# Performance work log

Hardware: AMD Instinct MI355X
Metric: run time of the kernel (lower is better)

Reference implementation:

```python
import jax, jax.numpy as jnp
import numpy as np

N = 100000      # nodes
E = 3200000     # edges (avg degree 32)
D = 256         # feature dim
C = 40          # classes
KEEP = 0.5      # 1 - dropout


def setup_inputs() -> dict:
    key = jax.random.key(0)
    k1, k2, k3, k4, k5, k6, k7 = jax.random.split(key, 7)
    x = jax.random.normal(k1, (N, D), dtype=jnp.float32)
    adj_row = jnp.sort(jax.random.randint(k2, (E,), 0, N))
    adj_col = jax.random.randint(k3, (E,), 0, N)
    # roughly degree-normalized edge weights (~1/avg_degree scale)
    adj_vals = jax.random.uniform(k4, (E,), dtype=jnp.float32) * (2.0 / 32.0)
    W = jax.random.normal(k5, (C, D), dtype=jnp.float32) * (1.0 / np.sqrt(D))
    b = jax.random.normal(k6, (C,), dtype=jnp.float32) * 0.01
    # precomputed dropout keep-mask (training mode, p=0.5)
    drop_mask = (jax.random.uniform(k7, (N, D)) < KEEP).astype(jnp.float32)
    return {"x": x, "adj_vals": adj_vals, "W": W, "b": b,
            "drop_mask": drop_mask, "adj_row": adj_row, "adj_col": adj_col}


def reference(x, adj_vals, W, b, drop_mask, adj_row, adj_col):
    n = x.shape[0]

    def spmm(v):  # sparse [N,N] @ dense [N,d] via gather + segment-sum
        return jax.ops.segment_sum(adj_vals[:, None] * v[adj_col], adj_row,
                                   num_segments=n)

    # hidden GraphConvolution (use_linear=False): spmm -> relu -> dropout
    h = jax.nn.relu(spmm(x))
    h = h * drop_mask / KEEP
    # gc_class: Linear(D->C) then spmm
    out = spmm(h @ W.T + b)  # [N, C]
    return out
```

## Files before the change

### kernel.cpp

```cpp
#include <hip/hip_runtime.h>

#define NN 100000
#define EE 3200000
#define DD 256
#define CC 40
#define NCH 8
#define CH 32
#define UN2 8

#define CAPW 640
#define COHORT 256
#define CHUNK_BLOCKS (COHORT * 8)
#define WPC (COHORT * 4)
#define WG16 (NN / 16)
#define LROWS 64

__device__ __forceinline__ float bf2f(unsigned int u) {
    return __uint_as_float(u << 16);
}
__device__ __forceinline__ unsigned short f2bf(float f) {
    unsigned int t = __float_as_uint(f);
    return (unsigned short)((t + 0x7FFFu + ((t >> 16) & 1u)) >> 16);
}

__global__ __launch_bounds__(256) void k_row_ptr(const int* __restrict__ adj_row,
                                                 int* __restrict__ row_ptr) {
    int e = blockIdx.x * 256 + threadIdx.x;
    if (e >= EE) return;
    int r = adj_row[e];
    int prev = (e == 0) ? -1 : adj_row[e - 1];
    for (int rr = prev + 1; rr <= r; ++rr) row_ptr[rr] = e;
    if (e == EE - 1) {
        for (int rr = r + 1; rr <= NN; ++rr) row_ptr[rr] = EE;
    }
}

__global__ __launch_bounds__(256) void k_cvt_t(const float* __restrict__ x,
                                               ushort* __restrict__ xb) {
    __shared__ ushort ls[32][DD + 4];
    int t = threadIdx.x;
    size_t r0 = (size_t)blockIdx.x * 32;
    const float4* src = (const float4*)(x + r0 * DD);
#pragma unroll
    for (int u = 0; u < 8; ++u) {
        int idx = u * 256 + t;
        float4 v = src[idx];
        int row = idx >> 6, d4 = idx & 63;
        ushort* p = &ls[row][d4 * 4];
        p[0] = f2bf(v.x); p[1] = f2bf(v.y); p[2] = f2bf(v.z); p[3] = f2bf(v.w);
    }
    __syncthreads();
    int c = t >> 5, r = t & 31;
    const uint4* s = (const uint4*)&ls[r][c * CH];
    uint4* dst = (uint4*)(xb + ((size_t)c * NN + r0 + r) * CH);
    dst[0] = s[0];
    dst[1] = s[1];
    dst[2] = s[2];
    dst[3] = s[3];
}

__global__ __launch_bounds__(256, 8) void k_chunk(
    const ushort* __restrict__ xb, const float* __restrict__ adj_vals,
    const int* __restrict__ adj_col, const int* __restrict__ row_ptr,
    const float* __restrict__ drop_mask, ushort* __restrict__ hb)
{
    __shared__ uint2 meta[4][CAPW];
    int bid = blockIdx.x;
    int c = bid & 7;
    int q = bid >> 3;
    int wave = threadIdx.x >> 6, lane = threadIdx.x & 63;
    int g = lane >> 2, i = lane & 3;
    const ushort* xc = xb + (size_t)c * NN * CH;
    uint2* mw = meta[wave];
    int gw0 = q * 4 + wave;

    for (int wg = gw0; wg < WG16; wg += WPC) {
        int row0 = wg * 16;
        int row  = row0 + g;
        int e_start = __builtin_amdgcn_readfirstlane(row_ptr[row0]);
        int e_end   = __builtin_amdgcn_readfirstlane(row_ptr[row0 + 16]);
        int nstage  = min(e_end - e_start, CAPW);

        for (int t = lane; t < nstage; t += 64) {
            uint2 m;
            m.x = (unsigned)adj_col[e_start + t];
            m.y = __float_as_uint(adj_vals[e_start + t]);
            mw[t] = m;
        }
        asm volatile("s_waitcnt lgkmcnt(0)" ::: "memory");
        __builtin_amdgcn_wave_barrier();

        int e0  = row_ptr[row];
        int cnt = row_ptr[row + 1] - e0;
        int eloc = e0 - e_start;
        float a0 = 0.f, a1 = 0.f, a2 = 0.f, a3 = 0.f;
        float a4 = 0.f, a5 = 0.f, a6 = 0.f, a7 = 0.f;

        if (eloc + cnt <= nstage) {
            int body = cnt & ~(UN2 - 1);
            int k = 0;
            for (; k < body; k += UN2) {
                uint2 mm[UN2];
#pragma unroll
                for (int u = 0; u < UN2; ++u) mm[u] = mw[eloc + k + u];
                uint4 xv[UN2];
#pragma unroll
                for (int u = 0; u < UN2; ++u)
                    xv[u] = *(const uint4*)(xc + (size_t)mm[u].x * CH + i * 8);
#pragma unroll
                for (int u = 0; u < UN2; ++u) {
                    float v = __uint_as_float(mm[u].y);
                    a0 = fmaf(v, bf2f(xv[u].x & 0xFFFFu), a0);
                    a1 = fmaf(v, bf2f(xv[u].x >> 16),     a1);
                    a2 = fmaf(v, bf2f(xv[u].y & 0xFFFFu), a2);
                    a3 = fmaf(v, bf2f(xv[u].y >> 16),     a3);
                    a4 = fmaf(v, bf2f(xv[u].z & 0xFFFFu), a4);
                    a5 = fmaf(v, bf2f(xv[u].z >> 16),     a5);
                    a6 = fmaf(v, bf2f(xv[u].w & 0xFFFFu), a6);
                    a7 = fmaf(v, bf2f(xv[u].w >> 16),     a7);
                }
            }
            if (k < cnt) {
#pragma unroll
                for (int u = 0; u < UN2; ++u) {
                    int kk = k + u;
                    uint2 m = mw[eloc + min(kk, cnt - 1)];
                    float v = (kk < cnt) ? __uint_as_float(m.y) : 0.f;
                    uint4 xv = *(const uint4*)(xc + (size_t)m.x * CH + i * 8);
                    a0 = fmaf(v, bf2f(xv.x & 0xFFFFu), a0);
                    a1 = fmaf(v, bf2f(xv.x >> 16),     a1);
                    a2 = fmaf(v, bf2f(xv.y & 0xFFFFu), a2);
                    a3 = fmaf(v, bf2f(xv.y >> 16),     a3);
                    a4 = fmaf(v, bf2f(xv.z & 0xFFFFu), a4);
                    a5 = fmaf(v, bf2f(xv.z >> 16),     a5);
                    a6 = fmaf(v, bf2f(xv.w & 0xFFFFu), a6);
                    a7 = fmaf(v, bf2f(xv.w >> 16),     a7);
                }
            }
        } else {
            for (int k = 0; k < cnt; ++k) {
                int idx = e0 + k;
                float v = adj_vals[idx];
                int col = adj_col[idx];
                uint4 xv = *(const uint4*)(xc + (size_t)col * CH + i * 8);
                a0 = fmaf(v, bf2f(xv.x & 0xFFFFu), a0);
                a1 = fmaf(v, bf2f(xv.x >> 16),     a1);
                a2 = fmaf(v, bf2f(xv.y & 0xFFFFu), a2);
                a3 = fmaf(v, bf2f(xv.y >> 16),     a3);
                a4 = fmaf(v, bf2f(xv.z & 0xFFFFu), a4);
                a5 = fmaf(v, bf2f(xv.z >> 16),     a5);
                a6 = fmaf(v, bf2f(xv.w & 0xFFFFu), a6);
                a7 = fmaf(v, bf2f(xv.w >> 16),     a7);
            }
        }
        __builtin_amdgcn_wave_barrier();

        {
            size_t off = (size_t)row * DD + c * CH + i * 8;
            const float* mp = drop_mask + off;
            float m0 = __builtin_nontemporal_load(mp);
            float m1 = __builtin_nontemporal_load(mp + 1);
            float m2 = __builtin_nontemporal_load(mp + 2);
            float m3 = __builtin_nontemporal_load(mp + 3);
            float m4 = __builtin_nontemporal_load(mp + 4);
            float m5 = __builtin_nontemporal_load(mp + 5);
            float m6 = __builtin_nontemporal_load(mp + 6);
            float m7 = __builtin_nontemporal_load(mp + 7);
            float h0 = fmaxf(a0, 0.f) * m0 * 2.f;
            float h1 = fmaxf(a1, 0.f) * m1 * 2.f;
            float h2 = fmaxf(a2, 0.f) * m2 * 2.f;
            float h3 = fmaxf(a3, 0.f) * m3 * 2.f;
            float h4 = fmaxf(a4, 0.f) * m4 * 2.f;
            float h5 = fmaxf(a5, 0.f) * m5 * 2.f;
            float h6 = fmaxf(a6, 0.f) * m6 * 2.f;
            float h7 = fmaxf(a7, 0.f) * m7 * 2.f;
            unsigned long long p0 =
                (unsigned long long)((unsigned)f2bf(h0) | ((unsigned)f2bf(h1) << 16)) |
                ((unsigned long long)((unsigned)f2bf(h2) | ((unsigned)f2bf(h3) << 16)) << 32);
            unsigned long long p1 =
                (unsigned long long)((unsigned)f2bf(h4) | ((unsigned)f2bf(h5) << 16)) |
                ((unsigned long long)((unsigned)f2bf(h6) | ((unsigned)f2bf(h7) << 16)) << 32);
            __builtin_nontemporal_store(p0, (unsigned long long*)(hb + off));
            __builtin_nontemporal_store(p1, (unsigned long long*)(hb + off + 4));
        }
    }
}

__global__ __launch_bounds__(256) void k_linear(
    const ushort* __restrict__ hb, const float* __restrict__ W,
    const float* __restrict__ b, ushort* __restrict__ z)
{
    __shared__ float ws[CC][DD + 4];
    int t = threadIdx.x;
    for (int idx = t; idx < CC * (DD / 4); idx += 256) {
        int c = idx >> 6, k4 = idx & 63;
        float4 v = ((const float4*)(W + (size_t)c * DD))[k4];
        float* p = &ws[c][k4 * 4];
        p[0] = v.x; p[1] = v.y; p[2] = v.z; p[3] = v.w;
    }
    __syncthreads();

    int row = blockIdx.x * LROWS + (t >> 2);
    int cg = (t & 3) * 10;
    if (row >= NN) return;

    const uint4* hrow = (const uint4*)(hb + (size_t)row * DD);
    float acc[10] = {0.f, 0.f, 0.f, 0.f, 0.f, 0.f, 0.f, 0.f, 0.f, 0.f};

    for (int k8 = 0; k8 < DD / 8; ++k8) {
        uint4 hv = hrow[k8];
        float h0 = bf2f(hv.x & 0xFFFFu), h1 = bf2f(hv.x >> 16);
        float h2 = bf2f(hv.y & 0xFFFFu), h3 = bf2f(hv.y >> 16);
        float h4 = bf2f(hv.z & 0xFFFFu), h5 = bf2f(hv.z >> 16);
        float h6 = bf2f(hv.w & 0xFFFFu), h7 = bf2f(hv.w >> 16);
#pragma unroll
        for (int j = 0; j < 10; ++j) {
            const float* wp = &ws[cg + j][k8 * 8];
            float4 wa = *(const float4*)wp;
            float4 wb = *(const float4*)(wp + 4);
            acc[j] = fmaf(h0, wa.x, fmaf(h1, wa.y,
                     fmaf(h2, wa.z, fmaf(h3, wa.w, acc[j]))));
            acc[j] = fmaf(h4, wb.x, fmaf(h5, wb.y,
                     fmaf(h6, wb.z, fmaf(h7, wb.w, acc[j]))));
        }
    }
#pragma unroll
    for (int j = 0; j < 10; ++j)
        z[(size_t)row * CC + cg + j] = f2bf(acc[j] + b[cg + j]);
}

__global__ __launch_bounds__(256) void k_spmm2(
    const ushort* __restrict__ z, const float* __restrict__ adj_vals,
    const int* __restrict__ adj_col, const int* __restrict__ row_ptr,
    float* __restrict__ out)
{
    int wave = threadIdx.x >> 6;
    int lane = threadIdx.x & 63;
    int row = blockIdx.x * 4 + wave;
    int cl = lane < CC ? lane : CC - 1;

    int e0 = __builtin_amdgcn_readfirstlane(row_ptr[row]);
    int e1 = __builtin_amdgcn_readfirstlane(row_ptr[row + 1]);

    float acc = 0.f;
    int nb = (e1 - e0 + UN2 - 1) / UN2;
    for (int bI = 0; bI < nb; ++bI) {
        int base = e0 + bI * UN2;
        float vv[UN2]; int cc[UN2];
#pragma unroll
        for (int u = 0; u < UN2; ++u) {
            int idx = base + u;
            bool ok = idx < e1;
            idx = ok ? idx : e1 - 1;
            vv[u] = ok ? adj_vals[idx] : 0.f;
            cc[u] = adj_col[idx];
        }
        float za[UN2];
#pragma unroll
        for (int u = 0; u < UN2; ++u)
            za[u] = bf2f((unsigned)z[(size_t)cc[u] * CC + cl]);
#pragma unroll
        for (int u = 0; u < UN2; ++u)
            acc = fmaf(vv[u], za[u], acc);
    }
    if (lane < CC) out[(size_t)row * CC + lane] = acc;
}

extern "C" void kernel_launch(void* const* d_in, const int* in_sizes, int n_in,
                              void* d_out, int out_size, void* d_ws, size_t ws_size,
                              hipStream_t stream) {
    const float* x         = (const float*)d_in[0];
    const float* adj_vals  = (const float*)d_in[1];
    const float* W         = (const float*)d_in[2];
    const float* b         = (const float*)d_in[3];
    const float* drop_mask = (const float*)d_in[4];
    const int*   adj_row   = (const int*)d_in[5];
    const int*   adj_col   = (const int*)d_in[6];
    float* out = (float*)d_out;

    char* wsp = (char*)d_ws;
    size_t rp_bytes = ((size_t)(NN + 1) * 4 + 255) & ~(size_t)255;
    size_t z_bytes  = (size_t)NN * CC * 4;
    size_t xb_bytes = (size_t)NN * DD * 2;
    int* row_ptr = (int*)wsp;
    ushort* zbuf = (ushort*)(wsp + rp_bytes);
    ushort* xb   = (ushort*)(wsp + rp_bytes + z_bytes);
    ushort* hb   = (ushort*)(wsp + rp_bytes + z_bytes + xb_bytes);

    hipLaunchKernelGGL(k_row_ptr, dim3((EE + 255) / 256), dim3(256), 0, stream,
                       adj_row, row_ptr);
    hipLaunchKernelGGL(k_cvt_t, dim3(NN / 32), dim3(256), 0, stream, x, xb);
    hipLaunchKernelGGL(k_chunk, dim3(CHUNK_BLOCKS), dim3(256), 0, stream,
                       xb, adj_vals, adj_col, row_ptr, drop_mask, hb);
    hipLaunchKernelGGL(k_linear, dim3((NN + LROWS - 1) / LROWS), dim3(256), 0,
                       stream, hb, W, b, zbuf);
    hipLaunchKernelGGL(k_spmm2, dim3(NN / 4), dim3(256), 0, stream,
                       zbuf, adj_vals, adj_col, row_ptr, out);
}
```

Before: 445.2 us.

## Prefetch next edge-group metadata in registers and pack dropout mask into bits

Measured after the change: 609.2 us. +36.8%, slower.

```diff
diff --git a/kernel.cpp b/kernel.cpp
--- a/kernel.cpp
+++ b/kernel.cpp
@@ -9,6 +9,7 @@
 #define UN2 8
 
 #define CAPW 640
+#define PF (CAPW / 64)
 #define COHORT 256
 #define CHUNK_BLOCKS (COHORT * 8)
 #define WPC (COHORT * 4)
@@ -36,7 +37,9 @@
 }
 
 __global__ __launch_bounds__(256) void k_cvt_t(const float* __restrict__ x,
-                                               ushort* __restrict__ xb) {
+                                               const float* __restrict__ drop_mask,
+                                               ushort* __restrict__ xb,
+                                               unsigned* __restrict__ mbits) {
     __shared__ ushort ls[32][DD + 4];
     int t = threadIdx.x;
     size_t r0 = (size_t)blockIdx.x * 32;
@@ -48,6 +51,20 @@
         int row = idx >> 6, d4 = idx & 63;
         ushort* p = &ls[row][d4 * 4];
         p[0] = f2bf(v.x); p[1] = f2bf(v.y); p[2] = f2bf(v.z); p[3] = f2bf(v.w);
+    }
+    {
+        int r = t >> 3, o = t & 7;
+        const float4* mp = (const float4*)(drop_mask + (r0 + r) * DD + o * 32);
+        unsigned bits = 0;
+#pragma unroll
+        for (int qq = 0; qq < 8; ++qq) {
+            float4 m = mp[qq];
+            bits |= (m.x != 0.f ? 1u : 0u) << (qq * 4 + 0);
+            bits |= (m.y != 0.f ? 1u : 0u) << (qq * 4 + 1);
+            bits |= (m.z != 0.f ? 1u : 0u) << (qq * 4 + 2);
+            bits |= (m.w != 0.f ? 1u : 0u) << (qq * 4 + 3);
+        }
+        mbits[(r0 + r) * 8 + o] = bits;
     }
     __syncthreads();
     int c = t >> 5, r = t & 31;
@@ -59,10 +76,10 @@
     dst[3] = s[3];
 }
 
-__global__ __launch_bounds__(256, 8) void k_chunk(
+__global__ __launch_bounds__(256, 7) void k_chunk(
     const ushort* __restrict__ xb, const float* __restrict__ adj_vals,
     const int* __restrict__ adj_col, const int* __restrict__ row_ptr,
-    const float* __restrict__ drop_mask, ushort* __restrict__ hb)
+    const unsigned* __restrict__ mbits, ushort* __restrict__ hb)
 {
     __shared__ uint2 meta[4][CAPW];
     int bid = blockIdx.x;
@@ -72,21 +89,48 @@
     int g = lane >> 2, i = lane & 3;
     const ushort* xc = xb + (size_t)c * NN * CH;
     uint2* mw = meta[wave];
-    int gw0 = q * 4 + wave;
-
-    for (int wg = gw0; wg < WG16; wg += WPC) {
+
+    int wg = q * 4 + wave;
+    if (wg >= WG16) return;
+
+    int es = __builtin_amdgcn_readfirstlane(row_ptr[wg * 16]);
+    int ee = __builtin_amdgcn_readfirstlane(row_ptr[wg * 16 + 16]);
+    int ns = min(ee - es, CAPW);
+    uint2 pf[PF];
+#pragma unroll
+    for (int j = 0; j < PF; ++j) {
+        int t = lane + 64 * j;
+        int idx = min(es + min(t, max(ns - 1, 0)), EE - 1);
+        pf[j].x = (unsigned)adj_col[idx];
+        pf[j].y = __float_as_uint(adj_vals[idx]);
+    }
+
+    while (true) {
         int row0 = wg * 16;
         int row  = row0 + g;
-        int e_start = __builtin_amdgcn_readfirstlane(row_ptr[row0]);
-        int e_end   = __builtin_amdgcn_readfirstlane(row_ptr[row0 + 16]);
-        int nstage  = min(e_end - e_start, CAPW);
-
-        for (int t = lane; t < nstage; t += 64) {
-            uint2 m;
-            m.x = (unsigned)adj_col[e_start + t];
-            m.y = __float_as_uint(adj_vals[e_start + t]);
-            mw[t] = m;
-        }
+        int e_start = es, nstage = ns;
+
+#pragma unroll
+        for (int j = 0; j < PF; ++j) {
+            int t = lane + 64 * j;
+            if (t < nstage) mw[t] = pf[j];
+        }
+
+        int wgn = wg + WPC;
+        bool more = wgn < WG16;
+        if (more) {
+            es = __builtin_amdgcn_readfirstlane(row_ptr[wgn * 16]);
+            ee = __builtin_amdgcn_readfirstlane(row_ptr[wgn * 16 + 16]);
+            ns = min(ee - es, CAPW);
+#pragma unroll
+            for (int j = 0; j < PF; ++j) {
+                int t = lane + 64 * j;
+                int idx = min(es + min(t, max(ns - 1, 0)), EE - 1);
+                pf[j].x = (unsigned)adj_col[idx];
+                pf[j].y = __float_as_uint(adj_vals[idx]);
+            }
+        }
+
         asm volatile("s_waitcnt lgkmcnt(0)" ::: "memory");
         __builtin_amdgcn_wave_barrier();
 
@@ -156,24 +200,17 @@
         __builtin_amdgcn_wave_barrier();
 
         {
+            unsigned mb = mbits[(size_t)row * 8 + c];
+            unsigned mbyte = (mb >> (i * 8)) & 0xFFu;
+            float h0 = (mbyte & 1u)   ? 2.f * fmaxf(a0, 0.f) : 0.f;
+            float h1 = (mbyte & 2u)   ? 2.f * fmaxf(a1, 0.f) : 0.f;
+            float h2 = (mbyte & 4u)   ? 2.f * fmaxf(a2, 0.f) : 0.f;
+            float h3 = (mbyte & 8u)   ? 2.f * fmaxf(a3, 0.f) : 0.f;
+            float h4 = (mbyte & 16u)  ? 2.f * fmaxf(a4, 0.f) : 0.f;
+            float h5 = (mbyte & 32u)  ? 2.f * fmaxf(a5, 0.f) : 0.f;
+            float h6 = (mbyte & 64u)  ? 2.f * fmaxf(a6, 0.f) : 0.f;
+            float h7 = (mbyte & 128u) ? 2.f * fmaxf(a7, 0.f) : 0.f;
             size_t off = (size_t)row * DD + c * CH + i * 8;
-            const float* mp = drop_mask + off;
-            float m0 = __builtin_nontemporal_load(mp);
-            float m1 = __builtin_nontemporal_load(mp + 1);
-            float m2 = __builtin_nontemporal_load(mp + 2);
-            float m3 = __builtin_nontemporal_load(mp + 3);
-            float m4 = __builtin_nontemporal_load(mp + 4);
-            float m5 = __builtin_nontemporal_load(mp + 5);
-            float m6 = __builtin_nontemporal_load(mp + 6);
-            float m7 = __builtin_nontemporal_load(mp + 7);
-            float h0 = fmaxf(a0, 0.f) * m0 * 2.f;
-            float h1 = fmaxf(a1, 0.f) * m1 * 2.f;
-            float h2 = fmaxf(a2, 0.f) * m2 * 2.f;
-            float h3 = fmaxf(a3, 0.f) * m3 * 2.f;
-            float h4 = fmaxf(a4, 0.f) * m4 * 2.f;
-            float h5 = fmaxf(a5, 0.f) * m5 * 2.f;
-            float h6 = fmaxf(a6, 0.f) * m6 * 2.f;
-            float h7 = fmaxf(a7, 0.f) * m7 * 2.f;
             unsigned long long p0 =
                 (unsigned long long)((unsigned)f2bf(h0) | ((unsigned)f2bf(h1) << 16)) |
                 ((unsigned long long)((unsigned)f2bf(h2) | ((unsigned)f2bf(h3) << 16)) << 32);
@@ -183,6 +220,9 @@
             __builtin_nontemporal_store(p0, (unsigned long long*)(hb + off));
             __builtin_nontemporal_store(p1, (unsigned long long*)(hb + off + 4));
         }
+
+        if (!more) break;
+        wg = wgn;
     }
 }
 
@@ -280,18 +320,21 @@
 
     char* wsp = (char*)d_ws;
     size_t rp_bytes = ((size_t)(NN + 1) * 4 + 255) & ~(size_t)255;
-    size_t z_bytes  = (size_t)NN * CC * 4;
+    size_t z_bytes  = (((size_t)NN * CC * 2) + 255) & ~(size_t)255;
     size_t xb_bytes = (size_t)NN * DD * 2;
-    int* row_ptr = (int*)wsp;
-    ushort* zbuf = (ushort*)(wsp + rp_bytes);
-    ushort* xb   = (ushort*)(wsp + rp_bytes + z_bytes);
-    ushort* hb   = (ushort*)(wsp + rp_bytes + z_bytes + xb_bytes);
+    size_t hb_bytes = (size_t)NN * DD * 2;
+    int* row_ptr    = (int*)wsp;
+    ushort* zbuf    = (ushort*)(wsp + rp_bytes);
+    ushort* xb      = (ushort*)(wsp + rp_bytes + z_bytes);
+    ushort* hb      = (ushort*)(wsp + rp_bytes + z_bytes + xb_bytes);
+    unsigned* mbits = (unsigned*)(wsp + rp_bytes + z_bytes + xb_bytes + hb_bytes);
 
     hipLaunchKernelGGL(k_row_ptr, dim3((EE + 255) / 256), dim3(256), 0, stream,
                        adj_row, row_ptr);
-    hipLaunchKernelGGL(k_cvt_t, dim3(NN / 32), dim3(256), 0, stream, x, xb);
+    hipLaunchKernelGGL(k_cvt_t, dim3(NN / 32), dim3(256), 0, stream,
+                       x, drop_mask, xb, mbits);
     hipLaunchKernelGGL(k_chunk, dim3(CHUNK_BLOCKS), dim3(256), 0, stream,
-                       xb, adj_vals, adj_col, row_ptr, drop_mask, hb);
+                       xb, adj_vals, adj_col, row_ptr, mbits, hb);
     hipLaunchKernelGGL(k_linear, dim3((NN + LROWS - 1) / LROWS), dim3(256), 0,
                        stream, hb, W, b, zbuf);
     hipLaunchKernelGGL(k_spmm2, dim3(NN / 4), dim3(256), 0, stream,
```
